# Kernel tuning notes

Measured on AMD Instinct MI355X. Metric: run time of the kernel, lower is better.

The kernel has to match this reference:

```python
import jax, jax.numpy as jnp
import numpy as np

BS, N, XC, K, YS = 64, 1024, 1024, 256, 768

def setup_inputs() -> dict:
    key = jax.random.key(0)
    ks = jax.random.split(key, 5)
    return {
        "x": jax.random.normal(ks[0], (BS, N, XC), dtype=jnp.float32),
        "y": jax.random.normal(ks[1], (BS, YS), dtype=jnp.float32),
        "W_ch": jax.random.normal(ks[2], (K, XC), dtype=jnp.float32) * 0.02,
        "b_ch": jax.random.normal(ks[3], (K,), dtype=jnp.float32) * 0.02,
        "W_y": jax.random.normal(ks[4], (K, YS), dtype=jnp.float32) * 0.02,
    }

def reference(x, y, W_ch, b_ch, W_y):
    # y_k: [bs, k] (no bias)
    y_k = jnp.einsum('bs,ks->bk', y, W_y)
    # channel affine on every spatial position, batched: [bs, n, k]
    x_k = jnp.einsum('bnc,kc->bnk', x, W_ch) + b_ch
    # add per-sample y_k (broadcast over spatial dim), tanh, softmax over k
    z = jnp.tanh(x_k + y_k[:, None, :])
    attn = jax.nn.softmax(z, axis=-1)
    # torch.cat over dim=0 of per-sample [n, k] blocks -> [bs*n, k]
    return attn.reshape(-1, attn.shape[-1])
```

## Files before the change

### kernel.cpp

```cpp
#include <hip/hip_runtime.h>


#define XC    1024
#define KOUT  256
#define LDSZ  65536

typedef float        f32x4_t  __attribute__((ext_vector_type(4)));
typedef unsigned int u32x4_t  __attribute__((ext_vector_type(4)));
typedef unsigned int u32x2_t  __attribute__((ext_vector_type(2)));
typedef __bf16       bf16x8_t __attribute__((ext_vector_type(8)));

__device__ __forceinline__ unsigned short f2bf(float f) {
  unsigned int u = __float_as_uint(f);
  u += 0x7fffu + ((u >> 16) & 1u);
  return (unsigned short)(u >> 16);
}

__device__ __forceinline__ unsigned int pack2bf(float a, float b) {
  unsigned int ua = __float_as_uint(a) + 0x8000u;
  unsigned int ub = __float_as_uint(b) + 0x8000u;
  return (ua >> 16) | (ub & 0xffff0000u);
}

__device__ __forceinline__ float fast_tanh(float v) {
  float e = __expf(2.0f * v);
  return 1.0f - 2.0f / (e + 1.0f);
}

__device__ __forceinline__ void async_copy16(void* lds, const void* g) {
  __builtin_amdgcn_global_load_lds(
      (const __attribute__((address_space(1))) void*)g,
      (__attribute__((address_space(3))) void*)lds, 16, 0, 0);
}

#define PIPE_WAIT_(N) asm volatile("s_waitcnt vmcnt(" #N ")" ::: "memory")
#define PIPE_WAIT(N)  PIPE_WAIT_(N)

__global__ void prep_kernel(const float* __restrict__ Wch,
                            const float* __restrict__ y,
                            const float* __restrict__ Wy,
                            const float* __restrict__ bch,
                            unsigned short* __restrict__ wbf,
                            float* __restrict__ biasws) {
  if (blockIdx.x < 256) {
    const int k = blockIdx.x;
    const int u = threadIdx.x;
    f32x4_t v = ((const f32x4_t*)(Wch + k * XC))[u];
    const int c0   = u << 2;
    const int t    = c0 >> 6;
    const int ch   = (c0 & 63) >> 3;
    const int kk   = ch >> 2;
    const int lg   = ch & 3;
    const int half = (c0 >> 2) & 1;
    const int wv   = k >> 6;
    const int ni   = (k >> 4) & 3;
    const int lr   = k & 15;
    const int lane = (lg << 4) | lr;
    unsigned int lo = (unsigned int)f2bf(v.x) | ((unsigned int)f2bf(v.y) << 16);
    unsigned int hi = (unsigned int)f2bf(v.z) | ((unsigned int)f2bf(v.w) << 16);
    char* p = (char*)wbf +
              ((size_t)((((t << 2) + wv) * 2 + kk) * 4 + ni) << 10) +
              (lane << 4) + (half << 3);
    *(u32x2_t*)p = (u32x2_t){lo, hi};
  } else {
    __shared__ __align__(16) float ys[768];
    const int b = blockIdx.x - 256;
    const int k = threadIdx.x;
    for (int i = k; i < 768; i += 256) ys[i] = y[b * 768 + i];
    __syncthreads();
    const f32x4_t* w4 = (const f32x4_t*)(Wy + k * 768);
    const f32x4_t* y4 = (const f32x4_t*)ys;
    float s = 0.f;
#pragma unroll 8
    for (int i = 0; i < 192; ++i) {
      f32x4_t w = w4[i], a = y4[i];
      s = fmaf(w.x, a.x, s); s = fmaf(w.y, a.y, s);
      s = fmaf(w.z, a.z, s); s = fmaf(w.w, a.w, s);
    }
    biasws[b * 256 + k] = s + bch[k];
  }
}

__global__ __launch_bounds__(256, 2) void fused_kernel(
    const float* __restrict__ x, const unsigned short* __restrict__ wbf,
    const float* __restrict__ bias, float* __restrict__ out) {
  __shared__ __align__(16) unsigned char smem[LDSZ];
  const int tid = threadIdx.x;
  const int l   = tid & 63;
  const int w   = tid >> 6;
  const int lr  = l & 15;
  const int lg  = l >> 4;
  const int m0  = blockIdx.x << 6;
  const int bidx = m0 >> 10;
  const int t0  = blockIdx.x & 15;

  f32x4_t acc[16];
#pragma unroll
  for (int i = 0; i < 16; ++i) acc[i] = (f32x4_t){0.f, 0.f, 0.f, 0.f};

  const char* xrow = (const char*)x +
      ((size_t)(m0 + (w << 4) + lr) << 12) + (lg << 5);
  const char* wsrc = (const char*)wbf;
  f32x4_t av0[2], av1[2], av2[2], av3[2];

#define LOADA(dst, s_) do {                                                  \
    const int off_ = (((((s_) >> 1) + t0) & 15) << 8) + (((s_) & 1) << 7);   \
    dst[0] = *(const f32x4_t*)(xrow + off_);                                 \
    dst[1] = *(const f32x4_t*)(xrow + off_ + 16);                            \
  } while (0)

#define DMAB(T_) do {                                                        \
    const int tile_ = ((T_) + t0) & 15;                                      \
    const char* g_ = wsrc + ((size_t)tile_ << 15) + (w << 13) + (l << 4);    \
    unsigned char* d_ = smem + (((T_) & 1) << 15) + (w << 13);               \
    _Pragma("unroll")                                                        \
    for (int i_ = 0; i_ < 8; ++i_)                                           \
      async_copy16(d_ + (i_ << 10), g_ + (i_ << 10));                        \
  } while (0)

#define PACK(avC)                                                            \
    u32x4_t afu_;                                                            \
    afu_[0] = pack2bf(avC[0].x, avC[0].y);                                   \
    afu_[1] = pack2bf(avC[0].z, avC[0].w);                                   \
    afu_[2] = pack2bf(avC[1].x, avC[1].y);                                   \
    afu_[3] = pack2bf(avC[1].z, avC[1].w);                                   \
    bf16x8_t afr_ = __builtin_bit_cast(bf16x8_t, afu_);

#define MFMAS(bufL, kkL) do {                                                \
    const u32x4_t* bB_ = (const u32x4_t*)(smem + ((bufL) << 15));            \
    _Pragma("unroll")                                                        \
    for (int wv2 = 0; wv2 < 4; ++wv2) {                                      \
      bf16x8_t bfr_[4];                                                      \
      _Pragma("unroll")                                                      \
      for (int ni = 0; ni < 4; ++ni)                                         \
        bfr_[ni] = __builtin_bit_cast(bf16x8_t,                              \
            bB_[(((((wv2 << 1) | (kkL)) << 2) | ni) << 6) + l]);             \
      _Pragma("unroll")                                                      \
      for (int ni = 0; ni < 4; ++ni)                                         \
        acc[(wv2 << 2) | ni] = __builtin_amdgcn_mfma_f32_16x16x32_bf16(      \
            afr_, bfr_[ni], acc[(wv2 << 2) | ni], 0, 0, 0);                  \
    }                                                                        \
  } while (0)

#define BARRIER(VM) do {                                                     \
    PIPE_WAIT(VM);                                                           \
    __builtin_amdgcn_s_barrier();                                            \
    __builtin_amdgcn_sched_barrier(0);                                       \
  } while (0)

#define STEPE(T_, avC, DODMA, DOLA) {                                        \
    if (DODMA) DMAB((T_) + 1);                                               \
    PACK(avC);                                                               \
    if (DOLA) LOADA(avC, 2 * (T_) + 4);                                      \
    MFMAS((T_) & 1, 0);                                                      \
  }
#define STEPO(T_, avC, DOLA, DOBAR, VM) {                                    \
    PACK(avC);                                                               \
    if (DOLA) LOADA(avC, 2 * (T_) + 5);                                      \
    MFMAS((T_) & 1, 1);                                                      \
    if (DOBAR) BARRIER(VM);                                                  \
  }

  DMAB(0);
  LOADA(av0, 0); LOADA(av1, 1); LOADA(av2, 2); LOADA(av3, 3);
  BARRIER(8);

  STEPE( 0, av0, 1, 1)  STEPO( 0, av1, 1, 1, 4)
  STEPE( 1, av2, 1, 1)  STEPO( 1, av3, 1, 1, 4)
  STEPE( 2, av0, 1, 1)  STEPO( 2, av1, 1, 1, 4)
  STEPE( 3, av2, 1, 1)  STEPO( 3, av3, 1, 1, 4)
  STEPE( 4, av0, 1, 1)  STEPO( 4, av1, 1, 1, 4)
  STEPE( 5, av2, 1, 1)  STEPO( 5, av3, 1, 1, 4)
  STEPE( 6, av0, 1, 1)  STEPO( 6, av1, 1, 1, 4)
  STEPE( 7, av2, 1, 1)  STEPO( 7, av3, 1, 1, 4)
  STEPE( 8, av0, 1, 1)  STEPO( 8, av1, 1, 1, 4)
  STEPE( 9, av2, 1, 1)  STEPO( 9, av3, 1, 1, 4)
  STEPE(10, av0, 1, 1)  STEPO(10, av1, 1, 1, 4)
  STEPE(11, av2, 1, 1)  STEPO(11, av3, 1, 1, 4)
  STEPE(12, av0, 1, 1)  STEPO(12, av1, 1, 1, 4)
  STEPE(13, av2, 1, 1)  STEPO(13, av3, 1, 1, 4)
  STEPE(14, av0, 1, 0)  STEPO(14, av1, 0, 1, 0)
  STEPE(15, av2, 0, 0)  STEPO(15, av3, 0, 0, 0)

#undef LOADA
#undef DMAB
#undef PACK
#undef MFMAS
#undef BARRIER
#undef STEPE
#undef STEPO

  float brow[16];
#pragma unroll
  for (int c = 0; c < 16; ++c)
    brow[c] = bias[(bidx << 8) + (c << 4) + lr];

#pragma unroll
  for (int c = 0; c < 16; ++c)
#pragma unroll
    for (int r = 0; r < 4; ++r)
      acc[c][r] = fast_tanh(acc[c][r] + brow[c]);

#pragma unroll
  for (int r = 0; r < 4; ++r) {
    float m = acc[0][r];
#pragma unroll
    for (int c = 1; c < 16; ++c) m = fmaxf(m, acc[c][r]);
    m = fmaxf(m, __shfl_xor(m, 1));
    m = fmaxf(m, __shfl_xor(m, 2));
    m = fmaxf(m, __shfl_xor(m, 4));
    m = fmaxf(m, __shfl_xor(m, 8));
    float ssum = 0.f;
#pragma unroll
    for (int c = 0; c < 16; ++c) {
      float e = __expf(acc[c][r] - m);
      acc[c][r] = e;
      ssum += e;
    }
    ssum += __shfl_xor(ssum, 1);
    ssum += __shfl_xor(ssum, 2);
    ssum += __shfl_xor(ssum, 4);
    ssum += __shfl_xor(ssum, 8);
    const float rinv = 1.0f / ssum;
    float* orow = out + ((size_t)(m0 + (w << 4) + (lg << 2) + r) << 8) + lr;
#pragma unroll
    for (int c = 0; c < 16; ++c)
      orow[c << 4] = acc[c][r] * rinv;
  }
}

extern "C" void kernel_launch(void* const* d_in, const int* in_sizes, int n_in,
                              void* d_out, int out_size, void* d_ws, size_t ws_size,
                              hipStream_t stream) {
  (void)in_sizes; (void)n_in; (void)out_size; (void)ws_size;
  const float* x   = (const float*)d_in[0];
  const float* y   = (const float*)d_in[1];
  const float* Wch = (const float*)d_in[2];
  const float* bch = (const float*)d_in[3];
  const float* Wy  = (const float*)d_in[4];
  float* out = (float*)d_out;
  unsigned short* wbf = (unsigned short*)d_ws;
  float* biasws = (float*)((char*)d_ws + 512 * 1024);

  hipLaunchKernelGGL(prep_kernel, dim3(320), dim3(256), 0, stream,
                     Wch, y, Wy, bch, wbf, biasws);
  hipLaunchKernelGGL(fused_kernel, dim3(1024), dim3(256), 0, stream,
                     x, wbf, biasws, out);
}
```

Baseline: 118.1 us.

## Drop LDS staging of weights, load B fragments from global, double rows per block

Removes the shared-memory double buffer and async global-to-LDS copies of the bf16 weight tiles. Each wave now reads its B fragments directly from global/L2 into registers. Each block covers 128 rows instead of 64 (two 16-row accumulator sets per wave), so every weight fragment feeds two MFMAs, and the grid is halved. Barriers disappear, but register pressure roughly doubles (32 accumulators plus 16 B fragments), which may cause spills or lower occupancy. Weight reads go through the cache with no explicit prefetch, and the smaller grid may underfill the GPU.

New measurement: 148.5 us. +25.7%, slower.

```diff
diff --git a/kernel.cpp b/kernel.cpp
--- a/kernel.cpp
+++ b/kernel.cpp
@@ -3,7 +3,6 @@
 
 #define XC    1024
 #define KOUT  256
-#define LDSZ  65536
 
 typedef float        f32x4_t  __attribute__((ext_vector_type(4)));
 typedef unsigned int u32x4_t  __attribute__((ext_vector_type(4)));
@@ -26,15 +25,6 @@
   float e = __expf(2.0f * v);
   return 1.0f - 2.0f / (e + 1.0f);
 }
-
-__device__ __forceinline__ void async_copy16(void* lds, const void* g) {
-  __builtin_amdgcn_global_load_lds(
-      (const __attribute__((address_space(1))) void*)g,
-      (__attribute__((address_space(3))) void*)lds, 16, 0, 0);
-}
-
-#define PIPE_WAIT_(N) asm volatile("s_waitcnt vmcnt(" #N ")" ::: "memory")
-#define PIPE_WAIT(N)  PIPE_WAIT_(N)
 
 __global__ void prep_kernel(const float* __restrict__ Wch,
                             const float* __restrict__ y,
@@ -84,149 +74,139 @@
 __global__ __launch_bounds__(256, 2) void fused_kernel(
     const float* __restrict__ x, const unsigned short* __restrict__ wbf,
     const float* __restrict__ bias, float* __restrict__ out) {
-  __shared__ __align__(16) unsigned char smem[LDSZ];
   const int tid = threadIdx.x;
   const int l   = tid & 63;
   const int w   = tid >> 6;
   const int lr  = l & 15;
   const int lg  = l >> 4;
-  const int m0  = blockIdx.x << 6;
+  const int m0  = blockIdx.x << 7;
   const int bidx = m0 >> 10;
   const int t0  = blockIdx.x & 15;
 
-  f32x4_t acc[16];
+  f32x4_t acc0[16], acc1[16];
 #pragma unroll
-  for (int i = 0; i < 16; ++i) acc[i] = (f32x4_t){0.f, 0.f, 0.f, 0.f};
-
-  const char* xrow = (const char*)x +
-      ((size_t)(m0 + (w << 4) + lr) << 12) + (lg << 5);
-  const char* wsrc = (const char*)wbf;
-  f32x4_t av0[2], av1[2], av2[2], av3[2];
-
-#define LOADA(dst, s_) do {                                                  \
+  for (int i = 0; i < 16; ++i) {
+    acc0[i] = (f32x4_t){0.f, 0.f, 0.f, 0.f};
+    acc1[i] = (f32x4_t){0.f, 0.f, 0.f, 0.f};
+  }
+
+  const char* xrow0 = (const char*)x +
+      ((size_t)(m0 + (w << 5) + lr) << 12) + (lg << 5);
+  const char* xrow1 = xrow0 + (16u << 12);
+  const char* wsrc  = (const char*)wbf + (l << 4);
+  f32x4_t avE0[2], avE1[2], avO0[2], avO1[2];
+
+#define LOADA2(d0, d1, s_) do {                                              \
     const int off_ = (((((s_) >> 1) + t0) & 15) << 8) + (((s_) & 1) << 7);   \
-    dst[0] = *(const f32x4_t*)(xrow + off_);                                 \
-    dst[1] = *(const f32x4_t*)(xrow + off_ + 16);                            \
+    d0[0] = *(const f32x4_t*)(xrow0 + off_);                                 \
+    d0[1] = *(const f32x4_t*)(xrow0 + off_ + 16);                            \
+    d1[0] = *(const f32x4_t*)(xrow1 + off_);                                 \
+    d1[1] = *(const f32x4_t*)(xrow1 + off_ + 16);                            \
   } while (0)
 
-#define DMAB(T_) do {                                                        \
-    const int tile_ = ((T_) + t0) & 15;                                      \
-    const char* g_ = wsrc + ((size_t)tile_ << 15) + (w << 13) + (l << 4);    \
-    unsigned char* d_ = smem + (((T_) & 1) << 15) + (w << 13);               \
-    _Pragma("unroll")                                                        \
-    for (int i_ = 0; i_ < 8; ++i_)                                           \
-      async_copy16(d_ + (i_ << 10), g_ + (i_ << 10));                        \
+#define PACK2(afr, avP)                                                      \
+    bf16x8_t afr; {                                                          \
+      u32x4_t u_;                                                            \
+      u_[0] = pack2bf(avP[0].x, avP[0].y);                                   \
+      u_[1] = pack2bf(avP[0].z, avP[0].w);                                   \
+      u_[2] = pack2bf(avP[1].x, avP[1].y);                                   \
+      u_[3] = pack2bf(avP[1].z, avP[1].w);                                   \
+      afr = __builtin_bit_cast(bf16x8_t, u_); }
+
+#define KSTEP(s_, aP0, aP1) do {                                             \
+    PACK2(afr0_, aP0)                                                        \
+    PACK2(afr1_, aP1)                                                        \
+    const char* bt_ = wsrc +                                                 \
+        ((size_t)((((s_) >> 1) + t0) & 15) << 15) + (((s_) & 1) << 12);      \
+    u32x4_t bf_[16];                                                         \
+    _Pragma("unroll")                                                        \
+    for (int g = 0; g < 4; ++g)                                              \
+      _Pragma("unroll")                                                      \
+      for (int ni = 0; ni < 4; ++ni)                                         \
+        bf_[(g << 2) | ni] =                                                 \
+            *(const u32x4_t*)(bt_ + (g << 13) + (ni << 10));                 \
+    if ((s_) + 2 < 32) LOADA2(aP0, aP1, (s_) + 2);                           \
+    _Pragma("unroll")                                                        \
+    for (int g = 0; g < 4; ++g)                                              \
+      _Pragma("unroll")                                                      \
+      for (int ni = 0; ni < 4; ++ni) {                                       \
+        const int c_ = (g << 2) | ni;                                        \
+        bf16x8_t bfr_ = __builtin_bit_cast(bf16x8_t, bf_[c_]);               \
+        acc0[c_] = __builtin_amdgcn_mfma_f32_16x16x32_bf16(                  \
+            afr0_, bfr_, acc0[c_], 0, 0, 0);                                 \
+        acc1[c_] = __builtin_amdgcn_mfma_f32_16x16x32_bf16(                  \
+            afr1_, bfr_, acc1[c_], 0, 0, 0);                                 \
+      }                                                                      \
   } while (0)
 
-#define PACK(avC)                                                            \
-    u32x4_t afu_;                                                            \
-    afu_[0] = pack2bf(avC[0].x, avC[0].y);                                   \
-    afu_[1] = pack2bf(avC[0].z, avC[0].w);                                   \
-    afu_[2] = pack2bf(avC[1].x, avC[1].y);                                   \
-    afu_[3] = pack2bf(avC[1].z, avC[1].w);                                   \
-    bf16x8_t afr_ = __builtin_bit_cast(bf16x8_t, afu_);
-
-#define MFMAS(bufL, kkL) do {                                                \
-    const u32x4_t* bB_ = (const u32x4_t*)(smem + ((bufL) << 15));            \
-    _Pragma("unroll")                                                        \
-    for (int wv2 = 0; wv2 < 4; ++wv2) {                                      \
-      bf16x8_t bfr_[4];                                                      \
-      _Pragma("unroll")                                                      \
-      for (int ni = 0; ni < 4; ++ni)                                         \
-        bfr_[ni] = __builtin_bit_cast(bf16x8_t,                              \
-            bB_[(((((wv2 << 1) | (kkL)) << 2) | ni) << 6) + l]);             \
-      _Pragma("unroll")                                                      \
-      for (int ni = 0; ni < 4; ++ni)                                         \
-        acc[(wv2 << 2) | ni] = __builtin_amdgcn_mfma_f32_16x16x32_bf16(      \
-            afr_, bfr_[ni], acc[(wv2 << 2) | ni], 0, 0, 0);                  \
-    }                                                                        \
-  } while (0)
-
-#define BARRIER(VM) do {                                                     \
-    PIPE_WAIT(VM);                                                           \
-    __builtin_amdgcn_s_barrier();                                            \
-    __builtin_amdgcn_sched_barrier(0);                                       \
-  } while (0)
-
-#define STEPE(T_, avC, DODMA, DOLA) {                                        \
-    if (DODMA) DMAB((T_) + 1);                                               \
-    PACK(avC);                                                               \
-    if (DOLA) LOADA(avC, 2 * (T_) + 4);                                      \
-    MFMAS((T_) & 1, 0);                                                      \
-  }
-#define STEPO(T_, avC, DOLA, DOBAR, VM) {                                    \
-    PACK(avC);                                                               \
-    if (DOLA) LOADA(avC, 2 * (T_) + 5);                                      \
-    MFMAS((T_) & 1, 1);                                                      \
-    if (DOBAR) BARRIER(VM);                                                  \
-  }
-
-  DMAB(0);
-  LOADA(av0, 0); LOADA(av1, 1); LOADA(av2, 2); LOADA(av3, 3);
-  BARRIER(8);
-
-  STEPE( 0, av0, 1, 1)  STEPO( 0, av1, 1, 1, 4)
-  STEPE( 1, av2, 1, 1)  STEPO( 1, av3, 1, 1, 4)
-  STEPE( 2, av0, 1, 1)  STEPO( 2, av1, 1, 1, 4)
-  STEPE( 3, av2, 1, 1)  STEPO( 3, av3, 1, 1, 4)
-  STEPE( 4, av0, 1, 1)  STEPO( 4, av1, 1, 1, 4)
-  STEPE( 5, av2, 1, 1)  STEPO( 5, av3, 1, 1, 4)
-  STEPE( 6, av0, 1, 1)  STEPO( 6, av1, 1, 1, 4)
-  STEPE( 7, av2, 1, 1)  STEPO( 7, av3, 1, 1, 4)
-  STEPE( 8, av0, 1, 1)  STEPO( 8, av1, 1, 1, 4)
-  STEPE( 9, av2, 1, 1)  STEPO( 9, av3, 1, 1, 4)
-  STEPE(10, av0, 1, 1)  STEPO(10, av1, 1, 1, 4)
-  STEPE(11, av2, 1, 1)  STEPO(11, av3, 1, 1, 4)
-  STEPE(12, av0, 1, 1)  STEPO(12, av1, 1, 1, 4)
-  STEPE(13, av2, 1, 1)  STEPO(13, av3, 1, 1, 4)
-  STEPE(14, av0, 1, 0)  STEPO(14, av1, 0, 1, 0)
-  STEPE(15, av2, 0, 0)  STEPO(15, av3, 0, 0, 0)
-
-#undef LOADA
-#undef DMAB
-#undef PACK
-#undef MFMAS
-#undef BARRIER
-#undef STEPE
-#undef STEPO
+  LOADA2(avE0, avE1, 0);
+  LOADA2(avO0, avO1, 1);
+
+  KSTEP( 0, avE0, avE1);  KSTEP( 1, avO0, avO1);
+  KSTEP( 2, avE0, avE1);  KSTEP( 3, avO0, avO1);
+  KSTEP( 4, avE0, avE1);  KSTEP( 5, avO0, avO1);
+  KSTEP( 6, avE0, avE1);  KSTEP( 7, avO0, avO1);
+  KSTEP( 8, avE0, avE1);  KSTEP( 9, avO0, avO1);
+  KSTEP(10, avE0, avE1);  KSTEP(11, avO0, avO1);
+  KSTEP(12, avE0, avE1);  KSTEP(13, avO0, avO1);
+  KSTEP(14, avE0, avE1);  KSTEP(15, avO0, avO1);
+  KSTEP(16, avE0, avE1);  KSTEP(17, avO0, avO1);
+  KSTEP(18, avE0, avE1);  KSTEP(19, avO0, avO1);
+  KSTEP(20, avE0, avE1);  KSTEP(21, avO0, avO1);
+  KSTEP(22, avE0, avE1);  KSTEP(23, avO0, avO1);
+  KSTEP(24, avE0, avE1);  KSTEP(25, avO0, avO1);
+  KSTEP(26, avE0, avE1);  KSTEP(27, avO0, avO1);
+  KSTEP(28, avE0, avE1);  KSTEP(29, avO0, avO1);
+  KSTEP(30, avE0, avE1);  KSTEP(31, avO0, avO1);
+
+#undef LOADA2
+#undef PACK2
+#undef KSTEP
 
   float brow[16];
 #pragma unroll
   for (int c = 0; c < 16; ++c)
     brow[c] = bias[(bidx << 8) + (c << 4) + lr];
 
-#pragma unroll
-  for (int c = 0; c < 16; ++c)
-#pragma unroll
-    for (int r = 0; r < 4; ++r)
-      acc[c][r] = fast_tanh(acc[c][r] + brow[c]);
-
-#pragma unroll
-  for (int r = 0; r < 4; ++r) {
-    float m = acc[0][r];
-#pragma unroll
-    for (int c = 1; c < 16; ++c) m = fmaxf(m, acc[c][r]);
-    m = fmaxf(m, __shfl_xor(m, 1));
-    m = fmaxf(m, __shfl_xor(m, 2));
-    m = fmaxf(m, __shfl_xor(m, 4));
-    m = fmaxf(m, __shfl_xor(m, 8));
-    float ssum = 0.f;
-#pragma unroll
-    for (int c = 0; c < 16; ++c) {
-      float e = __expf(acc[c][r] - m);
-      acc[c][r] = e;
-      ssum += e;
-    }
-    ssum += __shfl_xor(ssum, 1);
-    ssum += __shfl_xor(ssum, 2);
-    ssum += __shfl_xor(ssum, 4);
-    ssum += __shfl_xor(ssum, 8);
-    const float rinv = 1.0f / ssum;
-    float* orow = out + ((size_t)(m0 + (w << 4) + (lg << 2) + r) << 8) + lr;
-#pragma unroll
-    for (int c = 0; c < 16; ++c)
-      orow[c << 4] = acc[c][r] * rinv;
-  }
+#define EPI(accX, RFBASE) do {                                               \
+    _Pragma("unroll")                                                        \
+    for (int c = 0; c < 16; ++c)                                             \
+      _Pragma("unroll")                                                      \
+      for (int r = 0; r < 4; ++r)                                            \
+        accX[c][r] = fast_tanh(accX[c][r] + brow[c]);                        \
+    _Pragma("unroll")                                                        \
+    for (int r = 0; r < 4; ++r) {                                            \
+      float m = accX[0][r];                                                  \
+      _Pragma("unroll")                                                      \
+      for (int c = 1; c < 16; ++c) m = fmaxf(m, accX[c][r]);                 \
+      m = fmaxf(m, __shfl_xor(m, 1));                                        \
+      m = fmaxf(m, __shfl_xor(m, 2));                                        \
+      m = fmaxf(m, __shfl_xor(m, 4));                                        \
+      m = fmaxf(m, __shfl_xor(m, 8));                                        \
+      float ssum = 0.f;                                                      \
+      _Pragma("unroll")                                                      \
+      for (int c = 0; c < 16; ++c) {                                         \
+        float e = __expf(accX[c][r] - m);                                    \
+        accX[c][r] = e;                                                      \
+        ssum += e;                                                           \
+      }                                                                      \
+      ssum += __shfl_xor(ssum, 1);                                           \
+      ssum += __shfl_xor(ssum, 2);                                           \
+      ssum += __shfl_xor(ssum, 4);                                           \
+      ssum += __shfl_xor(ssum, 8);                                           \
+      const float rinv = 1.0f / ssum;                                        \
+      float* orow = out +                                                    \
+          ((size_t)(m0 + (w << 5) + (RFBASE) + (lg << 2) + r) << 8) + lr;    \
+      _Pragma("unroll")                                                      \
+      for (int c = 0; c < 16; ++c)                                           \
+        orow[c << 4] = accX[c][r] * rinv;                                    \
+    }                                                                        \
+  } while (0)
+
+  EPI(acc0, 0);
+  EPI(acc1, 16);
+
+#undef EPI
 }
 
 extern "C" void kernel_launch(void* const* d_in, const int* in_sizes, int n_in,
@@ -244,6 +224,6 @@
 
   hipLaunchKernelGGL(prep_kernel, dim3(320), dim3(256), 0, stream,
                      Wch, y, Wy, bch, wbf, biasws);
-  hipLaunchKernelGGL(fused_kernel, dim3(1024), dim3(256), 0, stream,
+  hipLaunchKernelGGL(fused_kernel, dim3(512), dim3(256), 0, stream,
                      x, wbf, biasws, out);
 }
```
